# Optimization experiments

Measured on AMD Instinct MI355X. Metric: run time of the kernel, lower is better.

## Reference

```python
import jax, jax.numpy as jnp
import numpy as np
from functools import reduce

N = 16          # total qubits
N_SQC = 4       # shadow-circuit qubits
BATCH = 512
DIM = 2 ** N    # 65536
CX = jnp.complex64


def multi_kron(mats):
    return reduce(jnp.kron, mats)


def ry(t):
    c = jnp.cos(t / 2).astype(CX)
    s = jnp.sin(t / 2).astype(CX)
    return jnp.stack([jnp.stack([c, -s]), jnp.stack([s, c])])


def rz(t):
    e = jnp.exp(-0.5j * t.astype(CX))
    z = jnp.zeros((), CX)
    return jnp.stack([jnp.stack([e, z]), jnp.stack([z, jnp.conj(e)])])


def yzy_layer(params, n):
    # per qubit i: apply Ry(p[3i]), Rz(p[3i+1]), Ry(p[3i+2]) -> u_i = Ry@Rz@Ry
    us = [ry(params[3 * i + 2]) @ rz(params[3 * i + 1]) @ ry(params[3 * i])
          for i in range(n)]
    return multi_kron(us)


def cnot(n, c, t):
    I = jnp.eye(2, dtype=CX)
    X = jnp.array([[0, 1], [1, 0]], dtype=CX)
    P0 = jnp.array([[1, 0], [0, 0]], dtype=CX)
    P1 = jnp.array([[0, 0], [0, 1]], dtype=CX)
    ops0 = [I] * n; ops0[c] = P0
    ops1 = [I] * n; ops1[c] = P1; ops1[t] = X
    return multi_kron(ops0) + multi_kron(ops1)


def ring_of_cnot(n):
    U = jnp.eye(2 ** n, dtype=CX)
    for i in range(n):  # CNOT(i, (i+1)%n) applied in order
        U = cnot(n, i, (i + 1) % n) @ U
    return U


def build_circuit(weight, n):
    # BasicEntangleLayer(repeat=2): [YZYLayer, ring_of_cnot] x 2, then final YZYLayer
    repeat = 2
    U = jnp.eye(2 ** n, dtype=CX)
    ring = ring_of_cnot(n)
    for r in range(repeat):
        U = yzy_layer(weight[3 * n * r:3 * n * (r + 1)], n) @ U
        U = ring @ U
    U = yzy_layer(weight[3 * n * repeat:3 * n * (repeat + 1)], n) @ U
    return U


def setup_inputs() -> dict:
    key = jax.random.key(0)
    k1, k2 = jax.random.split(key)
    vector_batch = jax.random.normal(k1, (BATCH, DIM), dtype=jnp.float32)
    weight = jax.random.uniform(k2, (9 * N_SQC,), dtype=jnp.float32,
                                minval=0.0, maxval=2.0 * np.pi)
    return {"vector_batch": vector_batch, "weight": weight}


def reference(vector_batch, weight):
    # row-wise L2 normalization + amplitude encoding (pad to 2**N), cast complex
    norm = jnp.sqrt(jnp.sum(vector_batch * vector_batch, axis=1, keepdims=True))
    state = (vector_batch / norm).astype(CX)
    state = jnp.pad(state, ((0, 0), (0, DIM - state.shape[1])))  # (B, 2^N)

    U = build_circuit(weight, N_SQC)                 # (2^n_sqc, 2^n_sqc)
    X = jnp.array([[0, 1], [1, 0]], dtype=CX)
    M = multi_kron([X] * N_SQC)                      # PauliX^{(x)n_sqc}
    T = U.conj().T @ M @ U                           # effective observable

    m = 2 ** N_SQC
    outs = []
    for start in range(N - N_SQC + 1):
        left = 2 ** start
        right = DIM // (left * m)
        # trace(rho * (I (x) T (x) I)) == <s| I (x) T (x) I |s>
        s = state.reshape(BATCH, left, m, right)
        y = jnp.einsum('ij,bajd->baid', T, s)
        o = jnp.einsum('baid,baid->b', jnp.conj(s), y).real
        outs.append(o)
    return jnp.stack(outs, axis=1).astype(jnp.float32)  # (B, N - n_sqc + 1)
```

## Files before the change

### kernel.cpp

```cpp
#include <hip/hip_runtime.h>
#include <math.h>


typedef _Float16 f16x8 __attribute__((ext_vector_type(8)));
typedef float f32x4 __attribute__((ext_vector_type(4)));
typedef float f32x16 __attribute__((ext_vector_type(16)));
#define MFMAH(a, b, c) __builtin_amdgcn_mfma_f32_16x16x32_f16((a), (b), (c), 0, 0, 0)
#define MFMA32(a, b, c) __builtin_amdgcn_mfma_f32_32x32x16_f16((a), (b), (c), 0, 0, 0)

union H4 { _Float16 h[4]; uint2 q; };
union Frag { _Float16 h[8]; f16x8 v; uint2 q[2]; unsigned int w[4]; };

__device__ __forceinline__ int swz(int g) { return g ^ (g >> 5); }

__device__ __forceinline__ float wave_sum(float x) {
    #pragma unroll
    for (int off = 32; off > 0; off >>= 1) x += __shfl_down(x, off, 64);
    return x;
}

using c2 = float2;
__device__ __forceinline__ c2 cmul(c2 a, c2 b) {
    return make_float2(a.x * b.x - a.y * b.y, a.x * b.y + a.y * b.x);
}
__device__ __forceinline__ c2 cadd(c2 a, c2 b) { return make_float2(a.x + b.x, a.y + b.y); }

__device__ __forceinline__ c2 kelem(const c2 u[4][2][2], int i, int j) {
    c2 p = cmul(u[0][(i >> 3) & 1][(j >> 3) & 1], u[1][(i >> 2) & 1][(j >> 2) & 1]);
    p = cmul(p, u[2][(i >> 1) & 1][(j >> 1) & 1]);
    p = cmul(p, u[3][i & 1][j & 1]);
    return p;
}
__device__ __forceinline__ int fperm(int x) {
    int b3 = (x >> 3) & 1, b2 = (x >> 2) & 1, b1 = (x >> 1) & 1, b0 = x & 1;
    b2 ^= b3; b1 ^= b2; b0 ^= b1; b3 ^= b0;
    return (b3 << 3) | (b2 << 2) | (b1 << 1) | b0;
}

__global__ __launch_bounds__(256) void setup_kernel(const float* __restrict__ weight,
                                                    float* __restrict__ ws) {
    __shared__ c2 ush[3][4][2][2];
    __shared__ c2 A[256], B[256];
    const int t = threadIdx.x;

    if (t < 12) {
        const int r = t / 4, q = t % 4;
        const float a = weight[12 * r + 3 * q + 0];
        const float b = weight[12 * r + 3 * q + 1];
        const float c = weight[12 * r + 3 * q + 2];
        const float ca = cosf(0.5f * a), sa = sinf(0.5f * a);
        const float cc = cosf(0.5f * c), sc = sinf(0.5f * c);
        const c2 e = make_float2(cosf(0.5f * b), -sinf(0.5f * b));
        const c2 eb = make_float2(e.x, -e.y);
        ush[r][q][0][0] = make_float2(cc * ca * e.x - sc * sa * eb.x, cc * ca * e.y - sc * sa * eb.y);
        ush[r][q][0][1] = make_float2(-cc * sa * e.x - sc * ca * eb.x, -cc * sa * e.y - sc * ca * eb.y);
        ush[r][q][1][0] = make_float2(sc * ca * e.x + cc * sa * eb.x, sc * ca * e.y + cc * sa * eb.y);
        ush[r][q][1][1] = make_float2(-sc * sa * e.x + cc * ca * eb.x, -sc * sa * e.y + cc * ca * eb.y);
    }
    __syncthreads();

    const int i = t >> 4, j = t & 15;
    A[t] = kelem(ush[0], i, j);
    __syncthreads();
    B[fperm(i) * 16 + j] = A[t];
    __syncthreads();
    {
        c2 acc = make_float2(0.f, 0.f);
        #pragma unroll
        for (int k = 0; k < 16; ++k) acc = cadd(acc, cmul(kelem(ush[1], i, k), B[k * 16 + j]));
        __syncthreads();
        A[t] = acc;
    }
    __syncthreads();
    B[fperm(i) * 16 + j] = A[t];
    __syncthreads();
    {
        c2 acc = make_float2(0.f, 0.f);
        #pragma unroll
        for (int k = 0; k < 16; ++k) acc = cadd(acc, cmul(kelem(ush[2], i, k), B[k * 16 + j]));
        __syncthreads();
        A[t] = acc;
    }
    __syncthreads();
    {
        float wr = 0.f;
        #pragma unroll
        for (int k = 0; k < 16; ++k) {
            const c2 a = A[k * 16 + i];
            const c2 b = A[(k ^ 15) * 16 + j];
            wr += a.x * b.x + a.y * b.y;
        }
        ws[t] = wr;
    }
    for (int z = t; z < 512 * 14; z += 256) ws[256 + z] = 0.f;
}


__device__ __forceinline__ void contract16(const float* __restrict__ Wl, const f32x4& acc,
                                           int i, int h, int l, float* dst) {
    const float4 wr = *(const float4*)&Wl[(i << 4) + (h << 2)];
    float q = wr.x * acc[0] + wr.y * acc[1] + wr.z * acc[2] + wr.w * acc[3];
    q = wave_sum(q);
    if (l == 0) atomicAdd(dst, q);
}

template <int S>
__device__ __forceinline__ void pair_unit(const unsigned short* __restrict__ sh16,
                                          const float* __restrict__ Wl,
                                          int l, float* accrow) {
    const int Jp = l & 31, h2 = l >> 5;
    f32x16 acc = {0.f, 0.f, 0.f, 0.f, 0.f, 0.f, 0.f, 0.f,
                  0.f, 0.f, 0.f, 0.f, 0.f, 0.f, 0.f, 0.f};
    #pragma unroll
    for (int cc = 0; cc < 16; ++cc) {
        int e0;
        if (S == 3)      e0 = (Jp << 8) + (cc << 4) + (h2 << 3);
        else if (S == 5) e0 = ((cc >> 2) << 11) + (Jp << 6) + ((cc & 3) << 4) + (h2 << 3);
        else             e0 = (cc << 9) + (Jp << 4) + (h2 << 3);
        const f16x8 f = *(const f16x8*)&sh16[swz(e0 >> 3) << 3];
        acc = MFMA32(f, f, acc);
    }
    float qa = 0.f, qb = 0.f;
    #pragma unroll
    for (int r2 = 0; r2 < 8; ++r2) {
        const int r = 2 * r2;
        const int J = (r & 3) + 8 * (r >> 2) + 4 * h2;
        const float w = Wl[((J >> 1) << 4) + (Jp >> 1)];
        qa += w * ((Jp & 1) ? acc[r + 1] : acc[r]);
    }
    #pragma unroll
    for (int r = 0; r < 8; ++r) {
        const int J = (r & 3) + 8 * (r >> 2) + 4 * h2;
        const float w = Wl[((J & 15) << 4) + (Jp & 15)];
        qb += w * ((Jp & 16) ? acc[r + 8] : acc[r]);
    }
    qa = wave_sum(qa);
    qb = wave_sum(qb);
    if (l == 0) { atomicAdd(&accrow[S], qa); atomicAdd(&accrow[S + 1], qb); }
}

__device__ __forceinline__ void unit9(const unsigned short* __restrict__ sh16,
                                      const float* __restrict__ Wl,
                                      int i, int h, int l, float* accrow) {
    f32x4 acc = {0.f, 0.f, 0.f, 0.f};
    #pragma unroll
    for (int cc = 0; cc < 16; ++cc) {
        const int e0 = ((4 * cc + h) << 7) + (i << 3);
        const f16x8 f = *(const f16x8*)&sh16[swz(e0 >> 3) << 3];
        acc = MFMAH(f, f, acc);
    }
    contract16(Wl, acc, i, h, l, &accrow[9]);
}

__device__ __forceinline__ void unit10(const unsigned short* __restrict__ sh16,
                                       const float* __restrict__ Wl,
                                       int i, int h, int l, int c0, int c1, float* accrow) {
    f32x4 acc = {0.f, 0.f, 0.f, 0.f};
    #pragma unroll
    for (int cc = c0; cc < c1; ++cc) {
        const int a0 = 8 * cc + 2 * h;
        const int ea = a0 * 64 + 4 * i;
        const int eb = ea + 64;
        Frag fr;
        fr.q[0] = *(const uint2*)&sh16[(swz(ea >> 3) << 3) + (ea & 7)];
        fr.q[1] = *(const uint2*)&sh16[(swz(eb >> 3) << 3) + (eb & 7)];
        acc = MFMAH(fr.v, fr.v, acc);
    }
    contract16(Wl, acc, i, h, l, &accrow[10]);
}

__device__ __forceinline__ void unit11(const unsigned short* __restrict__ sh16,
                                       const float* __restrict__ Wl,
                                       int i, int h, int l, int c0, int c1, float* accrow) {
    f32x4 acc = {0.f, 0.f, 0.f, 0.f};
    #pragma unroll
    for (int cc = c0; cc < c1; ++cc) {
        Frag fr;
        #pragma unroll
        for (int p = 0; p < 4; ++p) {
            const int ap = 16 * cc + 4 * h + p;
            const int e = ap * 32 + 2 * i;
            fr.w[p] = *(const unsigned int*)&sh16[(swz(e >> 3) << 3) + (e & 7)];
        }
        acc = MFMAH(fr.v, fr.v, acc);
    }
    contract16(Wl, acc, i, h, l, &accrow[11]);
}

__global__ __launch_bounds__(256, 5) void main_kernel(const float* __restrict__ v,
                                                      const float* __restrict__ ws,
                                                      float* __restrict__ accg) {
    __shared__ unsigned short sh16[8192];
    __shared__ float Wl[256];
    const int t = threadIdx.x;
    const int l = t & 63, wv = t >> 6;
    const int i = l & 15, h = l >> 4;
    Wl[t] = ws[t];

    if (blockIdx.x < 4096) {
        const int row = blockIdx.x >> 3, seg = blockIdx.x & 7;
        const float4* b4 = (const float4*)(v + ((size_t)row << 16) + (seg << 13));
        float* accrow = &accg[row * 14];

        float ss = 0.f;
        #pragma unroll
        for (int m = 0; m < 8; ++m) {
            const float4 d = b4[m * 256 + t];
            ss = fmaf(d.x, d.x, ss); ss = fmaf(d.y, d.y, ss);
            ss = fmaf(d.z, d.z, ss); ss = fmaf(d.w, d.w, ss);
            H4 p;
            p.h[0] = (_Float16)d.x; p.h[1] = (_Float16)d.y;
            p.h[2] = (_Float16)d.z; p.h[3] = (_Float16)d.w;
            const int e0 = (m * 256 + t) * 4;
            const int idx = (swz(e0 >> 3) << 3) + (e0 & 7);
            *(uint2*)&sh16[idx] = p.q;
        }
        {
            const float s2 = wave_sum(ss);
            if (l == 0) atomicAdd(&accrow[13], s2);
        }
        __syncthreads();

        if (wv == 0) {
            pair_unit<3>(sh16, Wl, l, accrow);
            unit10(sh16, Wl, i, h, l, 0, 8, accrow);
        } else if (wv == 1) {
            pair_unit<5>(sh16, Wl, l, accrow);
            unit10(sh16, Wl, i, h, l, 8, 16, accrow);
        } else if (wv == 2) {
            pair_unit<7>(sh16, Wl, l, accrow);
            unit11(sh16, Wl, i, h, l, 0, 8, accrow);
        } else {
            unit9(sh16, Wl, i, h, l, accrow);
            unit11(sh16, Wl, i, h, l, 8, 16, accrow);
        }
    } else {
        const int bi = blockIdx.x - 4096;
        const int row = bi >> 3;
        const int c0 = (bi & 7) << 6;
        const float* bp = v + ((size_t)row << 16) + c0 + l;
        float* accrow = &accg[row * 14];

        #pragma unroll
        for (int m = 0; m < 8; ++m) {
            const int u0 = 32 * wv + 4 * m;
            H4 p;
            p.h[0] = (_Float16)bp[(u0 + 0) * 512];
            p.h[1] = (_Float16)bp[(u0 + 1) * 512];
            p.h[2] = (_Float16)bp[(u0 + 2) * 512];
            p.h[3] = (_Float16)bp[(u0 + 3) * 512];
            *(uint2*)&sh16[l * 128 + (u0 ^ (8 * (l & 15)))] = p.q;
        }
        __syncthreads();

        if (wv == 0) {
            f32x4 acc = {0.f, 0.f, 0.f, 0.f};
            #pragma unroll
            for (int cc = 0; cc < 16; ++cc) {
                const int cl = 4 * cc + h;
                const f16x8 f = *(const f16x8*)&sh16[cl * 128 + ((8 * i) ^ (8 * (cl & 15)))];
                acc = MFMAH(f, f, acc);
            }
            contract16(Wl, acc, i, h, l, &accrow[0]);
        } else if (wv == 1) {
            {
                f32x4 acc = {0.f, 0.f, 0.f, 0.f};
                #pragma unroll
                for (int cc = 0; cc < 16; ++cc) {
                    const int cl = 4 * cc + h;
                    const int k = 8 * (cl & 15);
                    Frag fr;
                    fr.q[0] = *(const uint2*)&sh16[cl * 128 + ((4 * i) ^ k)];
                    fr.q[1] = *(const uint2*)&sh16[cl * 128 + ((64 + 4 * i) ^ k)];
                    acc = MFMAH(fr.v, fr.v, acc);
                }
                contract16(Wl, acc, i, h, l, &accrow[1]);
            }
            {
                f32x4 acc = {0.f, 0.f, 0.f, 0.f};
                #pragma unroll
                for (int cc = 12; cc < 16; ++cc) {
                    const int cl = 4 * cc + h;
                    const int k = 8 * (cl & 15);
                    Frag fr;
                    #pragma unroll
                    for (int p = 0; p < 4; ++p)
                        fr.w[p] = *(const unsigned int*)&sh16[cl * 128 + ((2 * i + 32 * p) ^ k)];
                    acc = MFMAH(fr.v, fr.v, acc);
                }
                contract16(Wl, acc, i, h, l, &accrow[2]);
            }
        } else if (wv == 2) {
            f32x4 acc = {0.f, 0.f, 0.f, 0.f};
            #pragma unroll
            for (int cc = 0; cc < 12; ++cc) {
                const int cl = 4 * cc + h;
                const int k = 8 * (cl & 15);
                Frag fr;
                #pragma unroll
                for (int p = 0; p < 4; ++p)
                    fr.w[p] = *(const unsigned int*)&sh16[cl * 128 + ((2 * i + 32 * p) ^ k)];
                acc = MFMAH(fr.v, fr.v, acc);
            }
            contract16(Wl, acc, i, h, l, &accrow[2]);
        } else {
            f32x4 acc = {0.f, 0.f, 0.f, 0.f};
            #pragma unroll
            for (int cc = 0; cc < 16; ++cc) {
                const int k0 = 32 * cc + 8 * h;
                const int cg = k0 >> 7, u0 = k0 & 127;
                const int col = 16 * cg + i;
                const f16x8 f = *(const f16x8*)&sh16[col * 128 + (u0 ^ (8 * i))];
                acc = MFMAH(f, f, acc);
            }
            contract16(Wl, acc, i, h, l, &accrow[12]);
        }
    }
}

__global__ __launch_bounds__(256) void finalize_kernel(const float* __restrict__ acc,
                                                       float* __restrict__ out) {
    const int idx = blockIdx.x * 256 + threadIdx.x;
    if (idx < 512 * 13) {
        const int row = idx / 13, s = idx % 13;
        out[idx] = acc[row * 14 + s] / acc[row * 14 + 13];
    }
}

extern "C" void kernel_launch(void* const* d_in, const int* in_sizes, int n_in,
                              void* d_out, int out_size, void* d_ws, size_t ws_size,
                              hipStream_t stream) {
    const float* vb = (const float*)d_in[0];
    const float* wt = (const float*)d_in[1];
    float* out = (float*)d_out;
    float* ws = (float*)d_ws;
    float* acc = ws + 256;

    setup_kernel<<<1, 256, 0, stream>>>(wt, ws);
    main_kernel<<<8192, 256, 0, stream>>>(vb, ws, acc);
    finalize_kernel<<<26, 256, 0, stream>>>(acc, out);
}
```

Baseline: 209.7 us.

## Fuse contiguous and strided work into persistent blocks with register-prefetch double buffering

Each block now handles two contiguous segments and two strided column tiles instead of one unit per block. The next unit's global loads go into registers while the current unit's MFMA compute runs, using two shared buffers that alternate. The grid shrinks from 8192 to 2048 blocks and the occupancy hint drops from 5 to 4 waves. The aim is to hide global memory latency behind compute, at the cost of more registers (32 floats plus 8 float4 per thread), double the LDS, and fewer blocks to balance across CUs.

```diff
diff --git a/kernel.cpp b/kernel.cpp
--- a/kernel.cpp
+++ b/kernel.cpp
@@ -187,134 +187,172 @@
     contract16(Wl, acc, i, h, l, &accrow[11]);
 }
 
-__global__ __launch_bounds__(256, 5) void main_kernel(const float* __restrict__ v,
+
+__device__ __forceinline__ void load_contig(const float* __restrict__ v, int cu, int t,
+                                            float4 (&rc)[8]) {
+    const float4* b4 = (const float4*)(v + ((size_t)(cu >> 3) << 16) + ((cu & 7) << 13));
+    #pragma unroll
+    for (int m = 0; m < 8; ++m) rc[m] = b4[m * 256 + t];
+}
+
+__device__ __forceinline__ void store_contig(const float4 (&rc)[8],
+                                             unsigned short* __restrict__ sh,
+                                             int t, int l, float* accrow) {
+    float ss = 0.f;
+    #pragma unroll
+    for (int m = 0; m < 8; ++m) {
+        const float4 d = rc[m];
+        ss = fmaf(d.x, d.x, ss); ss = fmaf(d.y, d.y, ss);
+        ss = fmaf(d.z, d.z, ss); ss = fmaf(d.w, d.w, ss);
+        H4 p;
+        p.h[0] = (_Float16)d.x; p.h[1] = (_Float16)d.y;
+        p.h[2] = (_Float16)d.z; p.h[3] = (_Float16)d.w;
+        const int e0 = (m * 256 + t) * 4;
+        const int idx = (swz(e0 >> 3) << 3) + (e0 & 7);
+        *(uint2*)&sh[idx] = p.q;
+    }
+    const float s2 = wave_sum(ss);
+    if (l == 0) atomicAdd(&accrow[13], s2);
+}
+
+__device__ __forceinline__ void load_col(const float* __restrict__ v, int du, int l, int wv,
+                                         float (&rl)[32]) {
+    const float* bp = v + ((size_t)(du >> 3) << 16) + ((du & 7) << 6) + l;
+    #pragma unroll
+    for (int q = 0; q < 32; ++q) rl[q] = bp[(32 * wv + q) * 512];
+}
+
+__device__ __forceinline__ void store_col(const float (&rl)[32],
+                                          unsigned short* __restrict__ sh,
+                                          int l, int wv) {
+    #pragma unroll
+    for (int m = 0; m < 8; ++m) {
+        const int u0 = 32 * wv + 4 * m;
+        H4 p;
+        p.h[0] = (_Float16)rl[4 * m + 0];
+        p.h[1] = (_Float16)rl[4 * m + 1];
+        p.h[2] = (_Float16)rl[4 * m + 2];
+        p.h[3] = (_Float16)rl[4 * m + 3];
+        *(uint2*)&sh[l * 128 + (u0 ^ (8 * (l & 15)))] = p.q;
+    }
+}
+
+__device__ __forceinline__ void compute_contig(const unsigned short* __restrict__ sh,
+                                               const float* __restrict__ Wl,
+                                               int wv, int i, int h, int l, float* accrow) {
+    if (wv == 0) {
+        pair_unit<3>(sh, Wl, l, accrow);
+        unit10(sh, Wl, i, h, l, 0, 8, accrow);
+    } else if (wv == 1) {
+        pair_unit<5>(sh, Wl, l, accrow);
+        unit10(sh, Wl, i, h, l, 8, 16, accrow);
+    } else if (wv == 2) {
+        pair_unit<7>(sh, Wl, l, accrow);
+        unit11(sh, Wl, i, h, l, 0, 8, accrow);
+    } else {
+        unit9(sh, Wl, i, h, l, accrow);
+        unit11(sh, Wl, i, h, l, 8, 16, accrow);
+    }
+}
+
+__device__ __forceinline__ void compute_col(const unsigned short* __restrict__ sh,
+                                            const float* __restrict__ Wl,
+                                            int wv, int i, int h, int l, float* accrow) {
+    if (wv == 0) {
+        f32x4 acc = {0.f, 0.f, 0.f, 0.f};
+        #pragma unroll
+        for (int cc = 0; cc < 16; ++cc) {
+            const int cl = 4 * cc + h;
+            const f16x8 f = *(const f16x8*)&sh[cl * 128 + ((8 * i) ^ (8 * (cl & 15)))];
+            acc = MFMAH(f, f, acc);
+        }
+        contract16(Wl, acc, i, h, l, &accrow[0]);
+    } else if (wv == 1) {
+        {
+            f32x4 acc = {0.f, 0.f, 0.f, 0.f};
+            #pragma unroll
+            for (int cc = 0; cc < 16; ++cc) {
+                const int cl = 4 * cc + h;
+                const int k = 8 * (cl & 15);
+                Frag fr;
+                fr.q[0] = *(const uint2*)&sh[cl * 128 + ((4 * i) ^ k)];
+                fr.q[1] = *(const uint2*)&sh[cl * 128 + ((64 + 4 * i) ^ k)];
+                acc = MFMAH(fr.v, fr.v, acc);
+            }
+            contract16(Wl, acc, i, h, l, &accrow[1]);
+        }
+        {
+            f32x4 acc = {0.f, 0.f, 0.f, 0.f};
+            #pragma unroll
+            for (int cc = 12; cc < 16; ++cc) {
+                const int cl = 4 * cc + h;
+                const int k = 8 * (cl & 15);
+                Frag fr;
+                #pragma unroll
+                for (int p = 0; p < 4; ++p)
+                    fr.w[p] = *(const unsigned int*)&sh[cl * 128 + ((2 * i + 32 * p) ^ k)];
+                acc = MFMAH(fr.v, fr.v, acc);
+            }
+            contract16(Wl, acc, i, h, l, &accrow[2]);
+        }
+    } else if (wv == 2) {
+        f32x4 acc = {0.f, 0.f, 0.f, 0.f};
+        #pragma unroll
+        for (int cc = 0; cc < 12; ++cc) {
+            const int cl = 4 * cc + h;
+            const int k = 8 * (cl & 15);
+            Frag fr;
+            #pragma unroll
+            for (int p = 0; p < 4; ++p)
+                fr.w[p] = *(const unsigned int*)&sh[cl * 128 + ((2 * i + 32 * p) ^ k)];
+            acc = MFMAH(fr.v, fr.v, acc);
+        }
+        contract16(Wl, acc, i, h, l, &accrow[2]);
+    } else {
+        f32x4 acc = {0.f, 0.f, 0.f, 0.f};
+        #pragma unroll
+        for (int cc = 0; cc < 16; ++cc) {
+            const int k0 = 32 * cc + 8 * h;
+            const int cg = k0 >> 7, u0 = k0 & 127;
+            const int col = 16 * cg + i;
+            const f16x8 f = *(const f16x8*)&sh[col * 128 + (u0 ^ (8 * i))];
+            acc = MFMAH(f, f, acc);
+        }
+        contract16(Wl, acc, i, h, l, &accrow[12]);
+    }
+}
+
+__global__ __launch_bounds__(256, 4) void main_kernel(const float* __restrict__ v,
                                                       const float* __restrict__ ws,
                                                       float* __restrict__ accg) {
-    __shared__ unsigned short sh16[8192];
+    __shared__ unsigned short shA[8192];
+    __shared__ unsigned short shB[8192];
     __shared__ float Wl[256];
     const int t = threadIdx.x;
     const int l = t & 63, wv = t >> 6;
     const int i = l & 15, h = l >> 4;
     Wl[t] = ws[t];
 
-    if (blockIdx.x < 4096) {
-        const int row = blockIdx.x >> 3, seg = blockIdx.x & 7;
-        const float4* b4 = (const float4*)(v + ((size_t)row << 16) + (seg << 13));
-        float* accrow = &accg[row * 14];
-
-        float ss = 0.f;
-        #pragma unroll
-        for (int m = 0; m < 8; ++m) {
-            const float4 d = b4[m * 256 + t];
-            ss = fmaf(d.x, d.x, ss); ss = fmaf(d.y, d.y, ss);
-            ss = fmaf(d.z, d.z, ss); ss = fmaf(d.w, d.w, ss);
-            H4 p;
-            p.h[0] = (_Float16)d.x; p.h[1] = (_Float16)d.y;
-            p.h[2] = (_Float16)d.z; p.h[3] = (_Float16)d.w;
-            const int e0 = (m * 256 + t) * 4;
-            const int idx = (swz(e0 >> 3) << 3) + (e0 & 7);
-            *(uint2*)&sh16[idx] = p.q;
-        }
-        {
-            const float s2 = wave_sum(ss);
-            if (l == 0) atomicAdd(&accrow[13], s2);
-        }
+    const int b = blockIdx.x;
+    float4 rc[8];
+    float rl[32];
+
+    load_contig(v, 2 * b, t, rc);
+    store_contig(rc, shA, t, l, &accg[((2 * b) >> 3) * 14]);
+    __syncthreads();
+
+    #pragma unroll
+    for (int p = 0; p < 2; ++p) {
+        const int cu = 2 * b + p;
+        const int du = 2 * b + p;
+        load_col(v, du, l, wv, rl);
+        compute_contig(shA, Wl, wv, i, h, l, &accg[(cu >> 3) * 14]);
+        store_col(rl, shB, l, wv);
         __syncthreads();
-
-        if (wv == 0) {
-            pair_unit<3>(sh16, Wl, l, accrow);
-            unit10(sh16, Wl, i, h, l, 0, 8, accrow);
-        } else if (wv == 1) {
-            pair_unit<5>(sh16, Wl, l, accrow);
-            unit10(sh16, Wl, i, h, l, 8, 16, accrow);
-        } else if (wv == 2) {
-            pair_unit<7>(sh16, Wl, l, accrow);
-            unit11(sh16, Wl, i, h, l, 0, 8, accrow);
-        } else {
-            unit9(sh16, Wl, i, h, l, accrow);
-            unit11(sh16, Wl, i, h, l, 8, 16, accrow);
-        }
-    } else {
-        const int bi = blockIdx.x - 4096;
-        const int row = bi >> 3;
-        const int c0 = (bi & 7) << 6;
-        const float* bp = v + ((size_t)row << 16) + c0 + l;
-        float* accrow = &accg[row * 14];
-
-        #pragma unroll
-        for (int m = 0; m < 8; ++m) {
-            const int u0 = 32 * wv + 4 * m;
-            H4 p;
-            p.h[0] = (_Float16)bp[(u0 + 0) * 512];
-            p.h[1] = (_Float16)bp[(u0 + 1) * 512];
-            p.h[2] = (_Float16)bp[(u0 + 2) * 512];
-            p.h[3] = (_Float16)bp[(u0 + 3) * 512];
-            *(uint2*)&sh16[l * 128 + (u0 ^ (8 * (l & 15)))] = p.q;
-        }
+        if (p == 0) load_contig(v, 2 * b + 1, t, rc);
+        compute_col(shB, Wl, wv, i, h, l, &accg[(du >> 3) * 14]);
+        if (p == 0) store_contig(rc, shA, t, l, &accg[((2 * b + 1) >> 3) * 14]);
         __syncthreads();
-
-        if (wv == 0) {
-            f32x4 acc = {0.f, 0.f, 0.f, 0.f};
-            #pragma unroll
-            for (int cc = 0; cc < 16; ++cc) {
-                const int cl = 4 * cc + h;
-                const f16x8 f = *(const f16x8*)&sh16[cl * 128 + ((8 * i) ^ (8 * (cl & 15)))];
-                acc = MFMAH(f, f, acc);
-            }
-            contract16(Wl, acc, i, h, l, &accrow[0]);
-        } else if (wv == 1) {
-            {
-                f32x4 acc = {0.f, 0.f, 0.f, 0.f};
-                #pragma unroll
-                for (int cc = 0; cc < 16; ++cc) {
-                    const int cl = 4 * cc + h;
-                    const int k = 8 * (cl & 15);
-                    Frag fr;
-                    fr.q[0] = *(const uint2*)&sh16[cl * 128 + ((4 * i) ^ k)];
-                    fr.q[1] = *(const uint2*)&sh16[cl * 128 + ((64 + 4 * i) ^ k)];
-                    acc = MFMAH(fr.v, fr.v, acc);
-                }
-                contract16(Wl, acc, i, h, l, &accrow[1]);
-            }
-            {
-                f32x4 acc = {0.f, 0.f, 0.f, 0.f};
-                #pragma unroll
-                for (int cc = 12; cc < 16; ++cc) {
-                    const int cl = 4 * cc + h;
-                    const int k = 8 * (cl & 15);
-                    Frag fr;
-                    #pragma unroll
-                    for (int p = 0; p < 4; ++p)
-                        fr.w[p] = *(const unsigned int*)&sh16[cl * 128 + ((2 * i + 32 * p) ^ k)];
-                    acc = MFMAH(fr.v, fr.v, acc);
-                }
-                contract16(Wl, acc, i, h, l, &accrow[2]);
-            }
-        } else if (wv == 2) {
-            f32x4 acc = {0.f, 0.f, 0.f, 0.f};
-            #pragma unroll
-            for (int cc = 0; cc < 12; ++cc) {
-                const int cl = 4 * cc + h;
-                const int k = 8 * (cl & 15);
-                Frag fr;
-                #pragma unroll
-                for (int p = 0; p < 4; ++p)
-                    fr.w[p] = *(const unsigned int*)&sh16[cl * 128 + ((2 * i + 32 * p) ^ k)];
-                acc = MFMAH(fr.v, fr.v, acc);
-            }
-            contract16(Wl, acc, i, h, l, &accrow[2]);
-        } else {
-            f32x4 acc = {0.f, 0.f, 0.f, 0.f};
-            #pragma unroll
-            for (int cc = 0; cc < 16; ++cc) {
-                const int k0 = 32 * cc + 8 * h;
-                const int cg = k0 >> 7, u0 = k0 & 127;
-                const int col = 16 * cg + i;
-                const f16x8 f = *(const f16x8*)&sh16[col * 128 + (u0 ^ (8 * i))];
-                acc = MFMAH(f, f, acc);
-            }
-            contract16(Wl, acc, i, h, l, &accrow[12]);
-        }
     }
 }
 
@@ -337,6 +375,6 @@
     float* acc = ws + 256;
 
     setup_kernel<<<1, 256, 0, stream>>>(wt, ws);
-    main_kernel<<<8192, 256, 0, stream>>>(vb, ws, acc);
+    main_kernel<<<2048, 256, 0, stream>>>(vb, ws, acc);
     finalize_kernel<<<26, 256, 0, stream>>>(acc, out);
 }
```

Result: slower. 460.8 us (+119.8%).
